# Kernel optimization log

Hardware: AMD Instinct MI355X
Metric: run time of the kernel (lower is better)

The kernel has to match this reference:

```python
import math
import jax, jax.numpy as jnp
import numpy as np

MODEL_DIM = 2048
NUM_HEADS = 16
HEAD_DIM = MODEL_DIM // NUM_HEADS
B, T = 4, 2048


def setup_inputs() -> dict:
    key = jax.random.key(0)
    ks = jax.random.split(key, 9)
    s = 0.02
    d = MODEL_DIM
    return {
        "x": jax.random.normal(ks[0], (B, T, d), dtype=jnp.float32),
        "wq": jax.random.normal(ks[1], (d, d), dtype=jnp.float32) * s,
        "bq": jnp.zeros((d,), dtype=jnp.float32),
        "wk": jax.random.normal(ks[2], (d, d), dtype=jnp.float32) * s,
        "bk": jnp.zeros((d,), dtype=jnp.float32),
        "wv": jax.random.normal(ks[3], (d, d), dtype=jnp.float32) * s,
        "bv": jnp.zeros((d,), dtype=jnp.float32),
        "wo": jax.random.normal(ks[4], (d, d), dtype=jnp.float32) * s,
        "bo": jnp.zeros((d,), dtype=jnp.float32),
    }


def reference(x, wq, bq, wk, bk, wv, bv, wo, bo):
    b, t, d = x.shape
    h, hd = NUM_HEADS, HEAD_DIM
    scale = 1.0 / math.sqrt(hd)
    # torch Linear: y = x @ W^T + b
    q = (x @ wq.T + bq).reshape(b, t, h, hd).transpose(0, 2, 1, 3)  # [B,H,T,hd]
    k = (x @ wk.T + bk).reshape(b, t, h, hd).transpose(0, 2, 1, 3)
    v = (x @ wv.T + bv).reshape(b, t, h, hd).transpose(0, 2, 1, 3)
    scores = jnp.einsum("bhqd,bhkd->bhqk", q, k) * scale  # [B,H,T,T]
    mask = jnp.tril(jnp.ones((t, t), dtype=bool))
    scores = jnp.where(mask[None, None], scores, -jnp.inf)
    probs = jax.nn.softmax(scores, axis=-1)
    out = jnp.einsum("bhqk,bhkd->bhqd", probs, v)  # [B,H,T,hd]
    out = out.transpose(0, 2, 1, 3).reshape(b, t, d)
    out = out @ wo.T + bo
    return (out, k, v)
```

## Files before the change

### kernel.cpp

```cpp
#include <hip/hip_runtime.h>
#include <hip/hip_bf16.h>
#include <stdint.h>

typedef __attribute__((ext_vector_type(8))) short short8;
typedef __attribute__((ext_vector_type(4))) float f32x4;

#define DEVI __device__ __forceinline__

DEVI unsigned short f2bf(float f) {
  union { float f; unsigned int u; } c; c.f = f;
  unsigned int u = c.u;
  u += 0x7fffu + ((u >> 16) & 1u);
  return (unsigned short)(u >> 16);
}

DEVI void gl_lds16(const void* gsrc, void* lds) {
  __builtin_amdgcn_global_load_lds(
      (const __attribute__((address_space(1))) unsigned int*)gsrc,
      (__attribute__((address_space(3))) unsigned int*)lds, 16, 0, 0);
}

#define MFMA(a, b, c) __builtin_amdgcn_mfma_f32_16x16x32_bf16((a), (b), (c), 0, 0, 0)
#define BAR()  __builtin_amdgcn_s_barrier()
#define SCHED0() __builtin_amdgcn_sched_barrier(0)

__global__ void cvt_f32_bf16(const float* __restrict__ in,
                             unsigned short* __restrict__ out, int n4) {
  const int stride = gridDim.x * blockDim.x;
  for (int i = blockIdx.x * blockDim.x + threadIdx.x; i < n4; i += stride) {
    const float4 v = ((const float4*)in)[i];
    ushort4 o;
    o.x = f2bf(v.x); o.y = f2bf(v.y); o.z = f2bf(v.z); o.w = f2bf(v.w);
    ((ushort4*)out)[i] = o;
  }
}


template<int MODE>
__global__ __launch_bounds__(512, 2)
void gemm8p(const unsigned short* __restrict__ A,
            const unsigned short* __restrict__ Bw,
            const float* __restrict__ bq,
            const float* __restrict__ bk,
            const float* __restrict__ bv,
            float* __restrict__ Kf,
            float* __restrict__ Vf,
            unsigned short* __restrict__ Qpk,
            unsigned short* __restrict__ Kpk,
            unsigned short* __restrict__ Vpk,
            float* __restrict__ Cf,
            int M, int N, int K)
{
  __shared__ unsigned short S[2][32768];
  const int tid  = threadIdx.x;
  const int lane = tid & 63;
  const int wid  = tid >> 6;
  const int l15  = lane & 15, l4 = lane >> 4;
  const int wm   = wid >> 2, wn = wid & 3;

  const int chunk = gridDim.x >> 3;
  const int q  = blockIdx.x;
  const int wg = (q & 7) * chunk + (q >> 3);
  const int bm = (wg & 31) * 256;
  const int bn = (wg >> 5) * 256;

  const unsigned short* Asrc = A  + (size_t)(bm + (wid >> 1) * 16 + l15) * K + (wid & 1) * 32 + l4 * 8;
  const unsigned short* Bsrc = Bw + (size_t)(bn + (wid >> 1) * 16 + l15) * K + (wid & 1) * 32 + l4 * 8;

  const int nKt   = K >> 6;
  const int HTmax = nKt * 4;

  auto stage_ht = [&](int g) {
    if (g >= HTmax) return;
    const int t = g >> 2, sub = g & 3, buf = t & 1, k0 = t << 6;
#pragma unroll
    for (int cc = 0; cc < 2; ++cc) {
      if (sub >= 2) {
        const int c = (sub - 2) * 2 + cc;
        gl_lds16(Asrc + (size_t)(c * 64) * K + k0,
                 &S[buf][c * 4096 + wid * 512 + lane * 8]);
      } else {
        const int c = sub * 2 + cc;
        gl_lds16(Bsrc + (size_t)(c * 64) * K + k0,
                 &S[buf][16384 + c * 4096 + wid * 512 + lane * 8]);
      }
    }
  };

#pragma unroll
  for (int g = 0; g < 7; ++g) stage_ht(g);
  asm volatile("s_waitcnt vmcnt(6)" ::: "memory");
  SCHED0();
  BAR();

  f32x4 acc[8][4] = {};
  short8 a[4][2], b[4][2];

  for (int t = 0; t < nKt; ++t) {
    const unsigned short* Sb = S[t & 1];
    const int P = t * 4;

#pragma unroll
    for (int i = 0; i < 4; ++i)
#pragma unroll
      for (int ks = 0; ks < 2; ++ks)
        a[i][ks] = *(const short8*)&Sb[((wm * 8 + i) * 2 + ks) * 512 + lane * 8];
#pragma unroll
    for (int j = 0; j < 4; ++j)
#pragma unroll
      for (int ks = 0; ks < 2; ++ks)
        b[j][ks] = *(const short8*)&Sb[16384 + ((wn * 4 + j) * 2 + ks) * 512 + lane * 8];
    stage_ht(P + 7);
    BAR();
    asm volatile("s_waitcnt lgkmcnt(0)" ::: "memory");
    SCHED0();
    __builtin_amdgcn_s_setprio(1);
#pragma unroll
    for (int i = 0; i < 4; ++i)
#pragma unroll
      for (int j = 0; j < 2; ++j)
#pragma unroll
        for (int ks = 0; ks < 2; ++ks)
          acc[i][j] = MFMA(a[i][ks], b[j][ks], acc[i][j]);
    __builtin_amdgcn_s_setprio(0);
    BAR();

    stage_ht(P + 8);
    BAR();
    __builtin_amdgcn_s_setprio(1);
#pragma unroll
    for (int i = 0; i < 4; ++i)
#pragma unroll
      for (int j = 0; j < 2; ++j)
#pragma unroll
        for (int ks = 0; ks < 2; ++ks)
          acc[i][2 + j] = MFMA(a[i][ks], b[2 + j][ks], acc[i][2 + j]);
    __builtin_amdgcn_s_setprio(0);
    BAR();

#pragma unroll
    for (int i = 0; i < 4; ++i)
#pragma unroll
      for (int ks = 0; ks < 2; ++ks)
        a[i][ks] = *(const short8*)&Sb[((wm * 8 + 4 + i) * 2 + ks) * 512 + lane * 8];
    stage_ht(P + 9);
    BAR();
    asm volatile("s_waitcnt lgkmcnt(0)" ::: "memory");
    SCHED0();
    __builtin_amdgcn_s_setprio(1);
#pragma unroll
    for (int i = 0; i < 4; ++i)
#pragma unroll
      for (int j = 0; j < 2; ++j)
#pragma unroll
        for (int ks = 0; ks < 2; ++ks)
          acc[4 + i][j] = MFMA(a[i][ks], b[j][ks], acc[4 + i][j]);
    __builtin_amdgcn_s_setprio(0);
    BAR();

    stage_ht(P + 10);
    if (t < nKt - 2)       { asm volatile("s_waitcnt vmcnt(6)" ::: "memory"); SCHED0(); }
    else if (t == nKt - 2) { asm volatile("s_waitcnt vmcnt(0)" ::: "memory"); SCHED0(); }
    BAR();
    __builtin_amdgcn_s_setprio(1);
#pragma unroll
    for (int i = 0; i < 4; ++i)
#pragma unroll
      for (int j = 0; j < 2; ++j)
#pragma unroll
        for (int ks = 0; ks < 2; ++ks)
          acc[4 + i][2 + j] = MFMA(a[i][ks], b[2 + j][ks], acc[4 + i][2 + j]);
    __builtin_amdgcn_s_setprio(0);
    BAR();
  }

  const int rbase = l4 * 4;
#pragma unroll
  for (int m = 0; m < 8; ++m) {
    const int row0 = bm + wm * 128 + m * 16 + rbase;
#pragma unroll
    for (int n = 0; n < 4; ++n) {
      const int col6 = bn + wn * 64 + n * 16 + l15;
      if constexpr (MODE == 3) {
        const float bb = bq[col6];
#pragma unroll
        for (int r = 0; r < 4; ++r)
          Cf[(size_t)(row0 + r) * N + col6] = acc[m][n][r] + bb;
      } else {
        const int sel = col6 >> 11;
        const int col = col6 & 2047;
        const float bb = (sel == 0 ? bq : sel == 1 ? bk : bv)[col];
        float vv[4];
#pragma unroll
        for (int r = 0; r < 4; ++r) vv[r] = acc[m][n][r] + bb;
        const int bI = row0 >> 11, t0 = row0 & 2047;
        const int h = col >> 7, e = col & 127;
        const size_t hb = ((size_t)(bI * 16 + h)) * 262144;
        if (sel == 0) {
          const size_t qb = hb + (size_t)(t0 >> 4) * 2048 + (e >> 5) * 512
                          + (t0 & 15) * 32 + (e & 31);
#pragma unroll
          for (int r = 0; r < 4; ++r) Qpk[qb + (size_t)r * 32] = f2bf(vv[r]);
        } else if (sel == 1) {
          const size_t idx = hb + (size_t)t0 * 128 + e;
          const size_t qb = hb + (size_t)(t0 >> 4) * 2048 + (e >> 5) * 512
                          + (t0 & 15) * 32 + (e & 31);
#pragma unroll
          for (int r = 0; r < 4; ++r) {
            Kf[idx + (size_t)r * 128] = vv[r];
            Kpk[qb + (size_t)r * 32] = f2bf(vv[r]);
          }
        } else {
          const size_t idx = hb + (size_t)t0 * 128 + e;
#pragma unroll
          for (int r = 0; r < 4; ++r) Vf[idx + (size_t)r * 128] = vv[r];
          const size_t vb = hb + (size_t)(t0 >> 6) * 8192 + (size_t)(e >> 4) * 1024
                          + ((t0 >> 5) & 1) * 512 + (e & 15) * 32 + (t0 & 31);
          ushort4 pk;
          pk.x = f2bf(vv[0]); pk.y = f2bf(vv[1]);
          pk.z = f2bf(vv[2]); pk.w = f2bf(vv[3]);
          *(ushort4*)&Vpk[vb] = pk;
        }
      }
    }
  }
}

__global__ __launch_bounds__(256, 2)
void attn_fwd(const unsigned short* __restrict__ Qf,
              const unsigned short* __restrict__ Kf,
              const unsigned short* __restrict__ Vf,
              unsigned short* __restrict__ Ab)
{
  constexpr float scale = 0.08838834764831843f;
  __shared__ unsigned short Pl[4][32][72];

  const int bid = blockIdx.x;
  const int idx = bid >> 3;
  const int bh  = (bid & 7) * 8 + (idx & 7);
  const int qb  = 15 - (idx >> 3);
  const int bI = bh >> 4, h = bh & 15;
  const int tid = threadIdx.x;
  const int wid = tid >> 6, lane = tid & 63;
  const int lr = lane & 15, lg = lane >> 4;
  const int lfo = lr * 32 + lg * 8;
  const int qw = qb * 128 + wid * 32;

  const unsigned short* Qp = Qf + (size_t)bh * 262144 + (size_t)(qw >> 4) * 2048;
  const unsigned short* Kp = Kf + (size_t)bh * 262144;
  const unsigned short* Vp = Vf + (size_t)bh * 262144;

  short8 qf[2][4];
#pragma unroll
  for (int m = 0; m < 2; ++m)
#pragma unroll
    for (int ks = 0; ks < 4; ++ks)
      qf[m][ks] = *(const short8*)&Qp[m * 2048 + ks * 512 + lfo];

  f32x4 o[2][8] = {};
  float mrun[2][4], lrun[2][4];
#pragma unroll
  for (int m = 0; m < 2; ++m)
#pragma unroll
    for (int r = 0; r < 4; ++r) { mrun[m][r] = -1e30f; lrun[m][r] = 0.f; }

  const int nfull = qw >> 6;
  for (int kt = 0; kt <= nfull; ++kt) {
    const int kv0 = kt * 64;
    const bool diag = (kt == nfull);
    const unsigned short* Kt = Kp + (size_t)(kv0 >> 4) * 2048;
    const unsigned short* Vt = Vp + (size_t)(kv0 >> 6) * 8192;

    short8 kf[4][4];
#pragma unroll
    for (int n = 0; n < 4; ++n)
#pragma unroll
      for (int ks = 0; ks < 4; ++ks)
        kf[n][ks] = *(const short8*)&Kt[n * 2048 + ks * 512 + lfo];
    f32x4 s[2][4] = {};
#pragma unroll
    for (int ks = 0; ks < 4; ++ks)
#pragma unroll
      for (int m = 0; m < 2; ++m)
#pragma unroll
        for (int n = 0; n < 4; ++n)
          s[m][n] = MFMA(qf[m][ks], kf[n][ks], s[m][n]);

    short8 vf[2][8];
#pragma unroll
    for (int ks2 = 0; ks2 < 2; ++ks2)
#pragma unroll
      for (int dt = 0; dt < 8; ++dt)
        vf[ks2][dt] = *(const short8*)&Vt[dt * 1024 + ks2 * 512 + lfo];

    float tmax[2][4];
#pragma unroll
    for (int m = 0; m < 2; ++m)
#pragma unroll
      for (int r = 0; r < 4; ++r) tmax[m][r] = -1e30f;
#pragma unroll
    for (int m = 0; m < 2; ++m)
#pragma unroll
      for (int n = 0; n < 4; ++n) {
        const int kg = kv0 + n * 16 + lr;
#pragma unroll
        for (int r = 0; r < 4; ++r) {
          float sv = s[m][n][r] * scale;
          if (diag) {
            const int qg = qw + m * 16 + lg * 4 + r;
            sv = (kg <= qg) ? sv : -1e30f;
          }
          s[m][n][r] = sv;
          tmax[m][r] = fmaxf(tmax[m][r], sv);
        }
      }
#pragma unroll
    for (int m = 0; m < 2; ++m)
#pragma unroll
      for (int r = 0; r < 4; ++r) {
#pragma unroll
        for (int off = 8; off >= 1; off >>= 1)
          tmax[m][r] = fmaxf(tmax[m][r], __shfl_xor(tmax[m][r], off));
        const float mnew  = fmaxf(mrun[m][r], tmax[m][r]);
        const float alpha = __expf(mrun[m][r] - mnew);
        mrun[m][r] = mnew;
        lrun[m][r] *= alpha;
#pragma unroll
        for (int d = 0; d < 8; ++d) o[m][d][r] *= alpha;
      }
#pragma unroll
    for (int m = 0; m < 2; ++m) {
      float ls[4] = {0.f, 0.f, 0.f, 0.f};
#pragma unroll
      for (int n = 0; n < 4; ++n)
#pragma unroll
        for (int r = 0; r < 4; ++r) {
          const float p = __expf(s[m][n][r] - mrun[m][r]);
          s[m][n][r] = p;
          ls[r] += p;
        }
#pragma unroll
      for (int r = 0; r < 4; ++r) {
#pragma unroll
        for (int off = 8; off >= 1; off >>= 1) ls[r] += __shfl_xor(ls[r], off);
        lrun[m][r] += ls[r];
      }
#pragma unroll
      for (int n = 0; n < 4; ++n)
#pragma unroll
        for (int r = 0; r < 4; ++r)
          Pl[wid][m * 16 + lg * 4 + r][n * 16 + lr] = f2bf(s[m][n][r]);
    }
#pragma unroll
    for (int ks2 = 0; ks2 < 2; ++ks2) {
      short8 pa[2];
#pragma unroll
      for (int m = 0; m < 2; ++m)
        pa[m] = *(const short8*)&Pl[wid][m * 16 + lr][ks2 * 32 + lg * 8];
#pragma unroll
      for (int dt = 0; dt < 8; ++dt)
#pragma unroll
        for (int m = 0; m < 2; ++m)
          o[m][dt] = MFMA(pa[m], vf[ks2][dt], o[m][dt]);
    }
  }
#pragma unroll
  for (int m = 0; m < 2; ++m)
#pragma unroll
    for (int r = 0; r < 4; ++r) {
      const float inv = 1.0f / lrun[m][r];
      const int t = qw + m * 16 + lg * 4 + r;
      unsigned short* dst = Ab + ((size_t)(bI * 2048 + t)) * 2048 + h * 128;
#pragma unroll
      for (int dt = 0; dt < 8; ++dt)
        dst[dt * 16 + lr] = f2bf(o[m][dt][r] * inv);
    }
}

extern "C" void kernel_launch(void* const* d_in, const int* in_sizes, int n_in,
                              void* d_out, int out_size, void* d_ws, size_t ws_size,
                              hipStream_t stream) {
  const float* x  = (const float*)d_in[0];
  const float* wq = (const float*)d_in[1];
  const float* bq = (const float*)d_in[2];
  const float* wk = (const float*)d_in[3];
  const float* bk = (const float*)d_in[4];
  const float* wv = (const float*)d_in[5];
  const float* bv = (const float*)d_in[6];
  const float* wo = (const float*)d_in[7];
  const float* bo = (const float*)d_in[8];

  float* out  = (float*)d_out;
  float* kout = out + (size_t)16777216;
  float* vout = out + (size_t)33554432;

  unsigned short* xb  = (unsigned short*)d_ws;
  unsigned short* wqb = xb  + 16777216;
  unsigned short* wkb = wqb + 4194304;
  unsigned short* wvb = wkb + 4194304;
  unsigned short* wob = wvb + 4194304;
  unsigned short* Qw  = wob + 4194304;
  unsigned short* Kw  = Qw  + 16777216;
  unsigned short* Vfw = Kw  + 16777216;
  unsigned short* Aw  = Vfw + 16777216;

  const int M = 8192, K = 2048;

  cvt_f32_bf16<<<1024, 256, 0, stream>>>(x,  xb,  4194304);
  cvt_f32_bf16<<<256,  256, 0, stream>>>(wq, wqb, 1048576);
  cvt_f32_bf16<<<256,  256, 0, stream>>>(wk, wkb, 1048576);
  cvt_f32_bf16<<<256,  256, 0, stream>>>(wv, wvb, 1048576);
  cvt_f32_bf16<<<256,  256, 0, stream>>>(wo, wob, 1048576);

  gemm8p<0><<<dim3(768), 512, 0, stream>>>(xb, wqb, bq, bk, bv,
                                           kout, vout, Qw, Kw, Vfw,
                                           nullptr, M, 6144, K);

  attn_fwd<<<dim3(1024), 256, 0, stream>>>(Qw, Kw, Vfw, Aw);

  gemm8p<3><<<dim3(256), 512, 0, stream>>>(Aw, wob, bo, nullptr, nullptr,
                                           nullptr, nullptr, nullptr, nullptr, nullptr,
                                           out, M, 2048, K);
}
```

Before: 552.9 us.

## Prefetch next K tile in attention, add MFMA priority, merge weight conversions

The attention loop now loads the next K tile into registers right after the QK^T MFMAs, so the global load latency overlaps with the softmax and PV work instead of stalling at the top of each iteration. s_setprio is raised around the MFMA blocks so a wave holds issue priority while it runs matrix ops. The four separate weight fp32-to-bf16 conversion launches are merged into one 2D-grid launch to cut launch overhead. The prefetch keeps more registers live, which could lower occupancy or cause spills.

```diff
diff --git a/kernel.cpp b/kernel.cpp
--- a/kernel.cpp
+++ b/kernel.cpp
@@ -26,6 +26,23 @@
 
 __global__ void cvt_f32_bf16(const float* __restrict__ in,
                              unsigned short* __restrict__ out, int n4) {
+  const int stride = gridDim.x * blockDim.x;
+  for (int i = blockIdx.x * blockDim.x + threadIdx.x; i < n4; i += stride) {
+    const float4 v = ((const float4*)in)[i];
+    ushort4 o;
+    o.x = f2bf(v.x); o.y = f2bf(v.y); o.z = f2bf(v.z); o.w = f2bf(v.w);
+    ((ushort4*)out)[i] = o;
+  }
+}
+
+__global__ void cvt_w4(const float* __restrict__ w0, const float* __restrict__ w1,
+                       const float* __restrict__ w2, const float* __restrict__ w3,
+                       unsigned short* __restrict__ o0, unsigned short* __restrict__ o1,
+                       unsigned short* __restrict__ o2, unsigned short* __restrict__ o3,
+                       int n4) {
+  const int sel = blockIdx.y;
+  const float* in = sel == 0 ? w0 : sel == 1 ? w1 : sel == 2 ? w2 : w3;
+  unsigned short* out = sel == 0 ? o0 : sel == 1 ? o1 : sel == 2 ? o2 : o3;
   const int stride = gridDim.x * blockDim.x;
   for (int i = blockIdx.x * blockDim.x + threadIdx.x; i < n4; i += stride) {
     const float4 v = ((const float4*)in)[i];
@@ -264,20 +281,21 @@
 #pragma unroll
     for (int r = 0; r < 4; ++r) { mrun[m][r] = -1e30f; lrun[m][r] = 0.f; }
 
+  short8 kf[4][4];
+#pragma unroll
+  for (int n = 0; n < 4; ++n)
+#pragma unroll
+    for (int ks = 0; ks < 4; ++ks)
+      kf[n][ks] = *(const short8*)&Kp[n * 2048 + ks * 512 + lfo];
+
   const int nfull = qw >> 6;
   for (int kt = 0; kt <= nfull; ++kt) {
     const int kv0 = kt * 64;
     const bool diag = (kt == nfull);
-    const unsigned short* Kt = Kp + (size_t)(kv0 >> 4) * 2048;
     const unsigned short* Vt = Vp + (size_t)(kv0 >> 6) * 8192;
 
-    short8 kf[4][4];
-#pragma unroll
-    for (int n = 0; n < 4; ++n)
-#pragma unroll
-      for (int ks = 0; ks < 4; ++ks)
-        kf[n][ks] = *(const short8*)&Kt[n * 2048 + ks * 512 + lfo];
     f32x4 s[2][4] = {};
+    __builtin_amdgcn_s_setprio(1);
 #pragma unroll
     for (int ks = 0; ks < 4; ++ks)
 #pragma unroll
@@ -285,6 +303,16 @@
 #pragma unroll
         for (int n = 0; n < 4; ++n)
           s[m][n] = MFMA(qf[m][ks], kf[n][ks], s[m][n]);
+    __builtin_amdgcn_s_setprio(0);
+
+    if (kt < nfull) {
+      const unsigned short* Kn = Kp + (size_t)((kv0 + 64) >> 4) * 2048;
+#pragma unroll
+      for (int n = 0; n < 4; ++n)
+#pragma unroll
+        for (int ks = 0; ks < 4; ++ks)
+          kf[n][ks] = *(const short8*)&Kn[n * 2048 + ks * 512 + lfo];
+    }
 
     short8 vf[2][8];
 #pragma unroll
@@ -357,11 +385,13 @@
 #pragma unroll
       for (int m = 0; m < 2; ++m)
         pa[m] = *(const short8*)&Pl[wid][m * 16 + lr][ks2 * 32 + lg * 8];
+      __builtin_amdgcn_s_setprio(1);
 #pragma unroll
       for (int dt = 0; dt < 8; ++dt)
 #pragma unroll
         for (int m = 0; m < 2; ++m)
           o[m][dt] = MFMA(pa[m], vf[ks2][dt], o[m][dt]);
+      __builtin_amdgcn_s_setprio(0);
     }
   }
 #pragma unroll
@@ -406,11 +436,9 @@
 
   const int M = 8192, K = 2048;
 
-  cvt_f32_bf16<<<1024, 256, 0, stream>>>(x,  xb,  4194304);
-  cvt_f32_bf16<<<256,  256, 0, stream>>>(wq, wqb, 1048576);
-  cvt_f32_bf16<<<256,  256, 0, stream>>>(wk, wkb, 1048576);
-  cvt_f32_bf16<<<256,  256, 0, stream>>>(wv, wvb, 1048576);
-  cvt_f32_bf16<<<256,  256, 0, stream>>>(wo, wob, 1048576);
+  cvt_f32_bf16<<<1024, 256, 0, stream>>>(x, xb, 4194304);
+  cvt_w4<<<dim3(256, 4), 256, 0, stream>>>(wq, wk, wv, wo,
+                                           wqb, wkb, wvb, wob, 1048576);
 
   gemm8p<0><<<dim3(768), 512, 0, stream>>>(xb, wqb, bq, bk, bv,
                                            kout, vout, Qw, Kw, Vfw,
```

Result: slower. 1.116 ms (+101.9%).
